# Kernel optimization log

Hardware: AMD Instinct MI355X
Metric: run time of the kernel (lower is better)

The kernel has to match this reference:

```python
import jax, jax.numpy as jnp
import numpy as np

HEADS, LEVELS, POINTS, DIMS = 8, 4, 4, 256
CH = DIMS // HEADS
SHAPES = np.array([[96, 96], [48, 48], [24, 24], [12, 12]], dtype=np.int64)
LEVEL_START = np.concatenate([[0], np.cumsum(SHAPES[:, 0] * SHAPES[:, 1])[:-1]]).astype(np.int64)
HW = int((SHAPES[:, 0] * SHAPES[:, 1]).sum())
N, Q = 2, HW


def setup_inputs() -> dict:
    key = jax.random.key(0)
    ks = jax.random.split(key, 8)
    return {
        "q": jax.random.normal(ks[0], (N, Q, DIMS), jnp.float32),
        "p": jax.random.uniform(ks[1], (N, Q, LEVELS, 2), jnp.float32),
        "v": jax.random.normal(ks[2], (N, HW, DIMS), jnp.float32),
        "W_off": jax.random.normal(ks[3], (DIMS, HEADS * LEVELS * POINTS * 2), jnp.float32) * 0.01,
        "b_off": jax.random.normal(ks[4], (HEADS * LEVELS * POINTS * 2,), jnp.float32) * 0.5,
        "W_attn": jax.random.normal(ks[5], (DIMS, HEADS * LEVELS * POINTS), jnp.float32) * 0.02,
        "b_attn": jnp.zeros((HEADS * LEVELS * POINTS,), jnp.float32),
        "W_in": jax.random.normal(ks[6], (DIMS, DIMS), jnp.float32) / np.float32(np.sqrt(DIMS)),
        "b_in": jnp.zeros((DIMS,), jnp.float32),
        "W_out": jax.random.normal(ks[7], (DIMS, DIMS), jnp.float32) / np.float32(np.sqrt(DIMS)),
        "b_out": jnp.zeros((DIMS,), jnp.float32),
        "shapes": jnp.asarray(SHAPES),
        "level_index": jnp.asarray(LEVEL_START),
    }


def _sample_level(vl, loc_l, Hl, Wl):
    """Bilinear sample with zero padding outside the feature map.
    vl: [N, Hl*Wl, heads, C]; loc_l: [N, Q, heads, P, 2] normalized (x, y) in [0,1].
    Returns [N, Q, P, heads, C]."""
    Nb, Qn, Hd, P, _ = loc_l.shape
    x = loc_l[..., 0] * Wl - 0.5  # pixel coords, align_corners=False convention
    y = loc_l[..., 1] * Hl - 0.5
    x0 = jnp.floor(x)
    y0 = jnp.floor(y)
    dx = x - x0
    dy = y - y0
    x0i = x0.astype(jnp.int32)
    y0i = y0.astype(jnp.int32)
    out = jnp.zeros((Nb, Qn, P, Hd, vl.shape[-1]), vl.dtype)
    corners = ((x0i, y0i, (1 - dx) * (1 - dy)), (x0i + 1, y0i, dx * (1 - dy)),
               (x0i, y0i + 1, (1 - dx) * dy), (x0i + 1, y0i + 1, dx * dy))
    for cx, cy, w in corners:
        valid = (cx >= 0) & (cx < Wl) & (cy >= 0) & (cy < Hl)
        idx = jnp.clip(cy, 0, Hl - 1) * Wl + jnp.clip(cx, 0, Wl - 1)  # [N,Q,Hd,P]
        idx_t = idx.transpose(0, 1, 3, 2).reshape(Nb, Qn * P, Hd, 1)
        g = jnp.take_along_axis(vl, idx_t, axis=1).reshape(Nb, Qn, P, Hd, -1)
        wv = jnp.where(valid, w, 0.0).transpose(0, 1, 3, 2)  # [N,Q,P,Hd]
        out = out + g * wv[..., None].astype(vl.dtype)
    return out


def _forward(q, p, v, W_off, b_off, W_attn, b_attn, W_in, b_in, W_out, b_out, shp, lsi):
    Nb, Qn, _ = q.shape
    v = (v @ W_in + b_in).reshape(Nb, -1, HEADS, CH)
    off = (q @ W_off + b_off).reshape(Nb, Qn, HEADS, LEVELS, POINTS, 2)
    attn = jax.nn.softmax((q @ W_attn + b_attn).reshape(Nb, Qn, HEADS, LEVELS * POINTS), axis=-1)
    attn = attn.reshape(Nb, Qn, HEADS, LEVELS, POINTS)
    # offsets normalized by (W, H) of each level, added to reference points (2-coord branch)
    off_norm = jnp.asarray(np.stack([shp[:, 1], shp[:, 0]], -1), q.dtype)  # [L, 2]
    loc = p[:, :, None, :, None, :] + off / off_norm[None, None, None, :, None, :]  # [N,Q,Hd,L,P,2]
    out = jnp.zeros((Nb, Qn, HEADS, CH), q.dtype)
    for l in range(LEVELS):
        Hl, Wl = int(shp[l, 0]), int(shp[l, 1])
        s = int(lsi[l])
        vl = jax.lax.slice_in_dim(v, s, s + Hl * Wl, axis=1)
        samp = _sample_level(vl, loc[:, :, :, l], Hl, Wl)  # [N,Q,P,Hd,C]
        out = out + jnp.einsum('nqphc,nqhp->nqhc', samp, attn[:, :, :, l])
    return out.reshape(Nb, Qn, DIMS) @ W_out + b_out


def reference(q, p, v, W_off, b_off, W_attn, b_attn, W_in, b_in, W_out, b_out, shapes, level_index):
    shp = np.asarray(shapes)  # spatial shapes are structural constants
    lsi = np.asarray(level_index)
    return _forward(q, p, v, W_off, b_off, W_attn, b_attn, W_in, b_in, W_out, b_out, shp, lsi)
```

## Files before the change

kernel.cpp:

```cpp
#include <hip/hip_runtime.h>
#include <hip/hip_bf16.h>
#include <hip/hip_fp16.h>
#include <math.h>

#define NB      2
#define QN      12240
#define HW_TOT  12240
#define DIMS    256
#define HEADS   8
#define CH      32
#define LEVELS  4
#define POINTS  4
#define M_TOT   (NB * QN)

typedef unsigned short ushort_t;
typedef __attribute__((ext_vector_type(8))) short short8;
typedef __attribute__((ext_vector_type(4))) float floatx4;

__device__ __forceinline__ ushort_t f2bf(float f) {
    __hip_bfloat16 h = __float2bfloat16(f);
    return *reinterpret_cast<ushort_t*>(&h);
}
__device__ __forceinline__ ushort_t f2h(float f) {
    __half h = __float2half(f);
    return *reinterpret_cast<ushort_t*>(&h);
}

__global__ __launch_bounds__(256) void convert_prep_kernel(
    const float* __restrict__ v, const float* __restrict__ q,
    ushort_t* __restrict__ vbf, ushort_t* __restrict__ qbf,
    const float* __restrict__ W_in, const float* __restrict__ W_off,
    const float* __restrict__ W_attn, const float* __restrict__ W_out,
    const float* __restrict__ b_off, const float* __restrict__ b_attn,
    ushort_t* __restrict__ Tin, ushort_t* __restrict__ Tcomb,
    ushort_t* __restrict__ Tout, float* __restrict__ bcomb,
    int* __restrict__ vpad)
{
    const int bx  = blockIdx.x;
    const int tid = threadIdx.x;
    if (bx < 6120) {
        const size_t i = ((size_t)bx * 256 + tid) * 8;
        const size_t half = (size_t)M_TOT * DIMS;
        const float* src; ushort_t* dst; size_t off;
        if (i < half) { src = v; dst = vbf; off = i; }
        else          { src = q; dst = qbf; off = i - half; }
        const float4 a = *(const float4*)&src[off];
        const float4 b = *(const float4*)&src[off + 4];
        ushort_t t[8] = {f2bf(a.x), f2bf(a.y), f2bf(a.z), f2bf(a.w),
                         f2bf(b.x), f2bf(b.y), f2bf(b.z), f2bf(b.w)};
        *(int4*)&dst[off] = *(int4*)t;
        return;
    }
    const int bi = bx - 6120;
    const int gi = bi * 256 + tid;
    if (gi < 32)  vpad[gi] = 0;
    if (gi < 384) bcomb[gi] = (gi < 256) ? b_off[gi] : b_attn[gi - 256];
    const int k = gi & 255;
    const int n = gi >> 8;
    if (gi < 65536) {
        Tin[n * 256 + k]  = f2bf(W_in[k * 256 + n]);
        Tout[n * 256 + k] = f2bf(W_out[k * 256 + n]);
    }
    {
        const float val = (n < 256) ? W_off[k * 256 + n]
                                    : W_attn[k * 128 + (n - 256)];
        Tcomb[n * 256 + k] = f2bf(val);
    }
}

__device__ __forceinline__ void gemm_tile_core(
    const ushort_t* __restrict__ A, const ushort_t* __restrict__ BT,
    const float* __restrict__ bias, void* __restrict__ C, int cmode,
    int M, int Nc, int bm0, int bn0, int K,
    ushort_t* As, ushort_t* Bs)
{
    const int tid  = threadIdx.x;
    const int wave = tid >> 6;
    const int lane = tid & 63;
    const int quad = lane >> 4;
    const int l16  = lane & 15;
    const int wm   = (wave >> 1) * 64;
    const int wn   = (wave & 1) * 64;

    const int off0 = tid * 16;
    const int row0 = off0 >> 6;
    const int kc0  = (off0 & 63) >> 1;

    int ar0 = bm0 + row0;      if (ar0 > M - 1) ar0 = M - 1;
    int ar1 = bm0 + row0 + 64; if (ar1 > M - 1) ar1 = M - 1;

    const ushort_t* ga0 = A  + (size_t)ar0 * K + kc0;
    const ushort_t* ga1 = A  + (size_t)ar1 * K + kc0;
    const ushort_t* gb0 = BT + (size_t)(bn0 + row0) * K + kc0;
    const ushort_t* gb1 = BT + (size_t)(bn0 + row0 + 64) * K + kc0;

    ushort_t* lA0 = As + wave * 512;
    ushort_t* lA1 = As + wave * 512 + 2048;
    ushort_t* lB0 = Bs + wave * 512;
    ushort_t* lB1 = Bs + wave * 512 + 2048;

    floatx4 acc[4][4];
    #pragma unroll
    for (int i = 0; i < 4; ++i)
        #pragma unroll
        for (int j = 0; j < 4; ++j)
            acc[i][j] = (floatx4){0.f, 0.f, 0.f, 0.f};

    for (int kk = 0; kk < K; kk += 32) {
        __builtin_amdgcn_global_load_lds(
            (const __attribute__((address_space(1))) void*)(ga0 + kk),
            (__attribute__((address_space(3))) void*)lA0, 16, 0, 0);
        __builtin_amdgcn_global_load_lds(
            (const __attribute__((address_space(1))) void*)(ga1 + kk),
            (__attribute__((address_space(3))) void*)lA1, 16, 0, 0);
        __builtin_amdgcn_global_load_lds(
            (const __attribute__((address_space(1))) void*)(gb0 + kk),
            (__attribute__((address_space(3))) void*)lB0, 16, 0, 0);
        __builtin_amdgcn_global_load_lds(
            (const __attribute__((address_space(1))) void*)(gb1 + kk),
            (__attribute__((address_space(3))) void*)lB1, 16, 0, 0);
        __syncthreads();

        short8 af[4], bfr[4];
        #pragma unroll
        for (int mt = 0; mt < 4; ++mt)
            af[mt] = *(const short8*)&As[(wm + mt * 16 + l16) * 32 + quad * 8];
        #pragma unroll
        for (int nt = 0; nt < 4; ++nt)
            bfr[nt] = *(const short8*)&Bs[(wn + nt * 16 + l16) * 32 + quad * 8];
        #pragma unroll
        for (int mt = 0; mt < 4; ++mt)
            #pragma unroll
            for (int nt = 0; nt < 4; ++nt)
                acc[mt][nt] = __builtin_amdgcn_mfma_f32_16x16x32_bf16(
                    af[mt], bfr[nt], acc[mt][nt], 0, 0, 0);
        __syncthreads();
    }

    #pragma unroll
    for (int mt = 0; mt < 4; ++mt) {
        #pragma unroll
        for (int j = 0; j < 4; ++j) {
            const int row = bm0 + wm + mt * 16 + quad * 4 + j;
            if (row >= M) continue;
            #pragma unroll
            for (int nt = 0; nt < 4; ++nt) {
                const int col = bn0 + wn + nt * 16 + l16;
                const float val = acc[mt][nt][j] + bias[col];
                if (cmode == 1) {
                    const size_t idx = (((size_t)(col >> 5) * M + row) << 5) + (col & 31);
                    ((ushort_t*)C)[idx] = f2bf(val);
                } else if (cmode == 2) {
                    ((ushort_t*)C)[(size_t)row * Nc + col] = f2h(val);
                } else {
                    ((float*)C)[(size_t)row * Nc + col] = val;
                }
            }
        }
    }
}

__global__ __launch_bounds__(256) void gemm_proj_kernel(
    const ushort_t* __restrict__ vbf, const ushort_t* __restrict__ qbf,
    const ushort_t* __restrict__ Tin, const ushort_t* __restrict__ Tcomb,
    const float* __restrict__ b_in, const float* __restrict__ bcomb,
    ushort_t* __restrict__ vproj, ushort_t* __restrict__ offh)
{
    __shared__ ushort_t As[128 * 32];
    __shared__ ushort_t Bs[128 * 32];
    const int bm0 = blockIdx.x * 128;
    const int y = blockIdx.y;
    if (y < 2)
        gemm_tile_core(vbf, Tin, b_in, vproj, 1, M_TOT, 256, bm0, y * 128, 256, As, Bs);
    else
        gemm_tile_core(qbf, Tcomb, bcomb, offh, 2, M_TOT, 384, bm0, (y - 2) * 128, 256, As, Bs);
}

__global__ __launch_bounds__(256) void gemm_out_kernel(
    const ushort_t* __restrict__ mid, const ushort_t* __restrict__ Tout,
    const float* __restrict__ b_out, float* __restrict__ out)
{
    __shared__ ushort_t As[128 * 32];
    __shared__ ushort_t Bs[128 * 32];
    gemm_tile_core(mid, Tout, b_out, out, 0, M_TOT, 256,
                   blockIdx.x * 128, blockIdx.y * 128, 256, As, Bs);
}

#define LO32(u) __uint_as_float((u) << 16)
#define HI32(u) __uint_as_float((u) & 0xffff0000u)
#define ACC8(W, g) \
    a0 = fmaf(W, LO32(g.x), a0);  a1 = fmaf(W, HI32(g.x), a1); \
    a2 = fmaf(W, LO32(g.y), a2);  a3 = fmaf(W, HI32(g.y), a3); \
    a4 = fmaf(W, LO32(g.z), a4);  a5 = fmaf(W, HI32(g.z), a5); \
    a6 = fmaf(W, LO32(g.w), a6);  a7 = fmaf(W, HI32(g.w), a7);

__global__ __launch_bounds__(256, 8) void msda_sample_kernel(
    const ushort_t* __restrict__ vproj, const ushort_t* __restrict__ offh,
    const float* __restrict__ p, ushort_t* __restrict__ mid)
{
    __shared__ int4 s_main[4][68];
    __shared__ int2 s_aux[4][68];

    const int tid = threadIdx.x;
    const int wv  = tid >> 6;
    const int l   = tid & 63;
    const int idx = blockIdx.x;
    const int b8  = idx & 7;
    const int hh  = b8 >> 2;
    const int qg  = (idx >> 3) * 4 + (b8 & 3);
    const int nq  = qg * 4 + wv;
    const int nb  = (nq >= QN) ? 1 : 0;

    const size_t orow = (size_t)nq * 384;
    const __half2 o2 = *(const __half2*)&offh[orow + hh * 128 + 2 * l];
    const float2  of = __half22float2(o2);
    const float   lg = __half2float(
        *(const __half*)&offh[orow + 256 + hh * 64 + l]);
    const int     lvl = (l >> 2) & 3;
    const float2  pl  = *(const float2*)&p[(size_t)nq * 8 + lvl * 2];

    float mx = lg;
    #pragma unroll
    for (int m = 8; m; m >>= 1) mx = fmaxf(mx, __shfl_xor(mx, m));
    const float e = __expf(lg - mx);
    float ss = e;
    #pragma unroll
    for (int m = 8; m; m >>= 1) ss += __shfl_xor(ss, m);
    const float wt = e * __builtin_amdgcn_rcpf(ss);

    const int   Wl = 96 >> lvl;
    const float fW = (float)Wl;
    const int   st = 12288 - (12288 >> (2 * lvl));
    const int   h4 = l >> 4;
    const int   h  = hh * 4 + h4;

    {
        const float x  = fmaf(pl.x, fW, of.x) - 0.5f;
        const float y  = fmaf(pl.y, fW, of.y) - 0.5f;
        const float xf = floorf(x), yf = floorf(y);
        const float dx = x - xf,    dy = y - yf;
        const int   x0 = (int)xf,   y0 = (int)yf;
        const bool vxl = (unsigned)x0       < (unsigned)Wl;
        const bool vxr = (unsigned)(x0 + 1) < (unsigned)Wl;
        const bool vy0 = (unsigned)y0       < (unsigned)Wl;
        const bool vy1 = (unsigned)(y0 + 1) < (unsigned)Wl;

        const float wxl = vxl ? (1.0f - dx) : (vxr ? dx : 0.0f);
        const float wxr = (vxl && vxr) ? dx : 0.0f;
        const int   xb  = vxl ? x0 : 0;

        const float wy0f = wt * (1.0f - dy), wy1f = wt * dy;
        const float w_l0 = vy0 ? wxl * wy0f : 0.0f;
        const float w_r0 = vy0 ? wxr * wy0f : 0.0f;
        const float w_l1 = vy1 ? wxl * wy1f : 0.0f;
        const float w_r1 = vy1 ? wxr * wy1f : 0.0f;

        int yc0 = y0;     if (yc0 < 0) yc0 = 0; if (yc0 > Wl - 1) yc0 = Wl - 1;
        int yc1 = y0 + 1; if (yc1 < 0) yc1 = 0; if (yc1 > Wl - 1) yc1 = Wl - 1;

        const int rowb = h * M_TOT + nb * HW_TOT + st + xb;
        const int lin0 = rowb + yc0 * Wl;
        const int lin1 = rowb + yc1 * Wl;
        const int e17 = h4 * 17 + (l & 15);
        s_main[wv][e17] = (int4){lin0 << 6, __float_as_int(w_l0),
                                 __float_as_int(w_r0), lin1 << 6};
        s_aux[wv][e17]  = (int2){__float_as_int(w_l1), __float_as_int(w_r1)};
    }

    __builtin_amdgcn_wave_barrier();
    asm volatile("s_waitcnt lgkmcnt(0)" ::: "memory");
    __builtin_amdgcn_wave_barrier();

    const int hg     = l >> 4;
    const int rowr   = (l >> 3) & 1;
    const int corner = (l >> 2) & 1;
    const int c16    = (l & 7) * 16;
    const char* __restrict__ vb = (const char*)vproj;

    float a0 = 0.f, a1 = 0.f, a2 = 0.f, a3 = 0.f;
    float a4 = 0.f, a5 = 0.f, a6 = 0.f, a7 = 0.f;

    #pragma unroll 4
    for (int t = 0; t < 16; ++t) {
        const int  e17 = hg * 17 + t;
        const int4 c   = s_main[wv][e17];
        const int2 cb  = s_aux[wv][e17];
        const int  base = rowr ? c.w : c.x;
        const float wl  = rowr ? __int_as_float(cb.x) : __int_as_float(c.y);
        const float wr  = rowr ? __int_as_float(cb.y) : __int_as_float(c.z);
        const float w   = corner ? wr : wl;
        const uint4 g   = *(const uint4*)(vb + (unsigned)(base + c16));
        ACC8(w, g);
    }

    a0 += __shfl_xor(a0, 4);  a1 += __shfl_xor(a1, 4);
    a2 += __shfl_xor(a2, 4);  a3 += __shfl_xor(a3, 4);
    a4 += __shfl_xor(a4, 4);  a5 += __shfl_xor(a5, 4);
    a6 += __shfl_xor(a6, 4);  a7 += __shfl_xor(a7, 4);
    a0 += __shfl_xor(a0, 8);  a1 += __shfl_xor(a1, 8);
    a2 += __shfl_xor(a2, 8);  a3 += __shfl_xor(a3, 8);
    a4 += __shfl_xor(a4, 8);  a5 += __shfl_xor(a5, 8);
    a6 += __shfl_xor(a6, 8);  a7 += __shfl_xor(a7, 8);

    if ((l & 12) == 0) {
        ushort_t mv[8] = {f2bf(a0), f2bf(a1), f2bf(a2), f2bf(a3),
                          f2bf(a4), f2bf(a5), f2bf(a6), f2bf(a7)};
        const int col = (hh * 4 + hg) * 32 + (l & 3) * 8;
        *(uint4*)&mid[(size_t)nq * 256 + col] = *(uint4*)mv;
    }
}

extern "C" void kernel_launch(void* const* d_in, const int* in_sizes, int n_in,
                              void* d_out, int out_size, void* d_ws, size_t ws_size,
                              hipStream_t stream)
{
    const float* q      = (const float*)d_in[0];
    const float* p      = (const float*)d_in[1];
    const float* v      = (const float*)d_in[2];
    const float* W_off  = (const float*)d_in[3];
    const float* b_off  = (const float*)d_in[4];
    const float* W_attn = (const float*)d_in[5];
    const float* b_attn = (const float*)d_in[6];
    const float* W_in   = (const float*)d_in[7];
    const float* b_in   = (const float*)d_in[8];
    const float* W_out  = (const float*)d_in[9];
    const float* b_out  = (const float*)d_in[10];
    float* out = (float*)d_out;

    const int M = M_TOT;

    ushort_t* vproj  = (ushort_t*)d_ws;
    ushort_t* vpad   = vproj + (size_t)M * 256;
    ushort_t* offh   = vpad + 64;
    ushort_t* vbf    = offh + (size_t)M * 384;
    ushort_t* mid    = vbf;
    ushort_t* qbf    = vbf + (size_t)M * 256;
    ushort_t* Tin    = qbf + (size_t)M * 256;
    ushort_t* Tcomb  = Tin + 256 * 256;
    ushort_t* Tout   = Tcomb + 384 * 256;
    float*    bcomb  = (float*)(Tout + 256 * 256);

    convert_prep_kernel<<<dim3(6504), 256, 0, stream>>>(
        v, q, vbf, qbf, W_in, W_off, W_attn, W_out, b_off, b_attn,
        Tin, Tcomb, Tout, bcomb, (int*)vpad);

    gemm_proj_kernel<<<dim3(192, 5), 256, 0, stream>>>(
        vbf, qbf, Tin, Tcomb, b_in, bcomb, vproj, offh);
    msda_sample_kernel<<<dim3(12240), 256, 0, stream>>>(vproj, offh, p, mid);
    gemm_out_kernel<<<dim3(192, 2), 256, 0, stream>>>(mid, Tout, b_out, out);
}
```

Measured before the change: 179.9 us.

## Fuse fp32-to-bf16 activation conversion into projection GEMM with dual-N tiles

Removes the separate pass that converted v and q to bf16 and instead loads fp32 activations directly in the projection GEMM, converting them in registers before writing them to LDS. Each block now also computes two 128-column N tiles from one converted A tile, so the A conversion and loads are shared across 256 output columns. This cuts a full write and reread of the bf16 copies and reduces the grid from 5 to 3 column groups. In exchange the fp32 A loads double the A read bytes per block and are synchronous register loads rather than async LDS loads, and the dual accumulators raise register pressure.

Measured after the change: 178.1 us. Within noise of the previous version (-1.0%).

```diff
diff --git a/kernel.cpp b/kernel.cpp
--- a/kernel.cpp
+++ b/kernel.cpp
@@ -26,9 +26,7 @@
     return *reinterpret_cast<ushort_t*>(&h);
 }
 
-__global__ __launch_bounds__(256) void convert_prep_kernel(
-    const float* __restrict__ v, const float* __restrict__ q,
-    ushort_t* __restrict__ vbf, ushort_t* __restrict__ qbf,
+__global__ __launch_bounds__(256) void prep_weights_kernel(
     const float* __restrict__ W_in, const float* __restrict__ W_off,
     const float* __restrict__ W_attn, const float* __restrict__ W_out,
     const float* __restrict__ b_off, const float* __restrict__ b_attn,
@@ -36,23 +34,7 @@
     ushort_t* __restrict__ Tout, float* __restrict__ bcomb,
     int* __restrict__ vpad)
 {
-    const int bx  = blockIdx.x;
-    const int tid = threadIdx.x;
-    if (bx < 6120) {
-        const size_t i = ((size_t)bx * 256 + tid) * 8;
-        const size_t half = (size_t)M_TOT * DIMS;
-        const float* src; ushort_t* dst; size_t off;
-        if (i < half) { src = v; dst = vbf; off = i; }
-        else          { src = q; dst = qbf; off = i - half; }
-        const float4 a = *(const float4*)&src[off];
-        const float4 b = *(const float4*)&src[off + 4];
-        ushort_t t[8] = {f2bf(a.x), f2bf(a.y), f2bf(a.z), f2bf(a.w),
-                         f2bf(b.x), f2bf(b.y), f2bf(b.z), f2bf(b.w)};
-        *(int4*)&dst[off] = *(int4*)t;
-        return;
-    }
-    const int bi = bx - 6120;
-    const int gi = bi * 256 + tid;
+    const int gi = blockIdx.x * 256 + threadIdx.x;
     if (gi < 32)  vpad[gi] = 0;
     if (gi < 384) bcomb[gi] = (gi < 256) ? b_off[gi] : b_attn[gi - 256];
     const int k = gi & 255;
@@ -61,18 +43,17 @@
         Tin[n * 256 + k]  = f2bf(W_in[k * 256 + n]);
         Tout[n * 256 + k] = f2bf(W_out[k * 256 + n]);
     }
-    {
-        const float val = (n < 256) ? W_off[k * 256 + n]
-                                    : W_attn[k * 128 + (n - 256)];
-        Tcomb[n * 256 + k] = f2bf(val);
-    }
-}
-
-__device__ __forceinline__ void gemm_tile_core(
-    const ushort_t* __restrict__ A, const ushort_t* __restrict__ BT,
-    const float* __restrict__ bias, void* __restrict__ C, int cmode,
-    int M, int Nc, int bm0, int bn0, int K,
-    ushort_t* As, ushort_t* Bs)
+    const float val = (n < 256) ? W_off[k * 256 + n]
+                                : W_attn[k * 128 + (n - 256)];
+    Tcomb[n * 256 + k] = f2bf(val);
+}
+
+template<int CMODE, bool DUAL>
+__device__ __forceinline__ void gemm_fused_tile(
+    const float* __restrict__ A32, const ushort_t* __restrict__ BT,
+    const float* __restrict__ bias, void* __restrict__ C,
+    int M, int Nc, int bm0, int bn0a, int bn0b,
+    ushort_t* As, ushort_t* Bs0, ushort_t* Bs1)
 {
     const int tid  = threadIdx.x;
     const int wave = tid >> 6;
@@ -89,6 +70,152 @@
     int ar0 = bm0 + row0;      if (ar0 > M - 1) ar0 = M - 1;
     int ar1 = bm0 + row0 + 64; if (ar1 > M - 1) ar1 = M - 1;
 
+    const float*    gA0  = A32 + (size_t)ar0 * 256 + kc0;
+    const float*    gA1  = A32 + (size_t)ar1 * 256 + kc0;
+    const ushort_t* gb0a = BT + (size_t)(bn0a + row0) * 256 + kc0;
+    const ushort_t* gb1a = BT + (size_t)(bn0a + row0 + 64) * 256 + kc0;
+    const ushort_t* gb0b = BT + (size_t)(bn0b + row0) * 256 + kc0;
+    const ushort_t* gb1b = BT + (size_t)(bn0b + row0 + 64) * 256 + kc0;
+
+    ushort_t* lB0a = Bs0 + wave * 512;
+    ushort_t* lB1a = Bs0 + wave * 512 + 2048;
+    ushort_t* lB0b = Bs1 + wave * 512;
+    ushort_t* lB1b = Bs1 + wave * 512 + 2048;
+
+    floatx4 acc0[4][4], acc1[4][4];
+    #pragma unroll
+    for (int i = 0; i < 4; ++i)
+        #pragma unroll
+        for (int j = 0; j < 4; ++j) {
+            acc0[i][j] = (floatx4){0.f, 0.f, 0.f, 0.f};
+            if (DUAL) acc1[i][j] = (floatx4){0.f, 0.f, 0.f, 0.f};
+        }
+
+    for (int kk = 0; kk < 256; kk += 32) {
+        __builtin_amdgcn_global_load_lds(
+            (const __attribute__((address_space(1))) void*)(gb0a + kk),
+            (__attribute__((address_space(3))) void*)lB0a, 16, 0, 0);
+        __builtin_amdgcn_global_load_lds(
+            (const __attribute__((address_space(1))) void*)(gb1a + kk),
+            (__attribute__((address_space(3))) void*)lB1a, 16, 0, 0);
+        if (DUAL) {
+            __builtin_amdgcn_global_load_lds(
+                (const __attribute__((address_space(1))) void*)(gb0b + kk),
+                (__attribute__((address_space(3))) void*)lB0b, 16, 0, 0);
+            __builtin_amdgcn_global_load_lds(
+                (const __attribute__((address_space(1))) void*)(gb1b + kk),
+                (__attribute__((address_space(3))) void*)lB1b, 16, 0, 0);
+        }
+        {
+            const float4 a0 = *(const float4*)(gA0 + kk);
+            const float4 a1 = *(const float4*)(gA0 + kk + 4);
+            const float4 b0 = *(const float4*)(gA1 + kk);
+            const float4 b1 = *(const float4*)(gA1 + kk + 4);
+            ushort_t t0[8] = {f2bf(a0.x), f2bf(a0.y), f2bf(a0.z), f2bf(a0.w),
+                              f2bf(a1.x), f2bf(a1.y), f2bf(a1.z), f2bf(a1.w)};
+            ushort_t t1[8] = {f2bf(b0.x), f2bf(b0.y), f2bf(b0.z), f2bf(b0.w),
+                              f2bf(b1.x), f2bf(b1.y), f2bf(b1.z), f2bf(b1.w)};
+            *(int4*)&As[tid * 8]        = *(int4*)t0;
+            *(int4*)&As[tid * 8 + 2048] = *(int4*)t1;
+        }
+        __syncthreads();
+
+        short8 af[4], bfa[4], bfb[4];
+        #pragma unroll
+        for (int mt = 0; mt < 4; ++mt)
+            af[mt] = *(const short8*)&As[(wm + mt * 16 + l16) * 32 + quad * 8];
+        #pragma unroll
+        for (int nt = 0; nt < 4; ++nt) {
+            bfa[nt] = *(const short8*)&Bs0[(wn + nt * 16 + l16) * 32 + quad * 8];
+            if (DUAL)
+                bfb[nt] = *(const short8*)&Bs1[(wn + nt * 16 + l16) * 32 + quad * 8];
+        }
+        #pragma unroll
+        for (int mt = 0; mt < 4; ++mt)
+            #pragma unroll
+            for (int nt = 0; nt < 4; ++nt) {
+                acc0[mt][nt] = __builtin_amdgcn_mfma_f32_16x16x32_bf16(
+                    af[mt], bfa[nt], acc0[mt][nt], 0, 0, 0);
+                if (DUAL)
+                    acc1[mt][nt] = __builtin_amdgcn_mfma_f32_16x16x32_bf16(
+                        af[mt], bfb[nt], acc1[mt][nt], 0, 0, 0);
+            }
+        __syncthreads();
+    }
+
+    #pragma unroll
+    for (int mt = 0; mt < 4; ++mt) {
+        #pragma unroll
+        for (int j = 0; j < 4; ++j) {
+            const int row = bm0 + wm + mt * 16 + quad * 4 + j;
+            if (row >= M) continue;
+            #pragma unroll
+            for (int nt = 0; nt < 4; ++nt) {
+                {
+                    const int col = bn0a + wn + nt * 16 + l16;
+                    const float val = acc0[mt][nt][j] + bias[col];
+                    if (CMODE == 1) {
+                        const size_t idx = (((size_t)(col >> 5) * M + row) << 5) + (col & 31);
+                        ((ushort_t*)C)[idx] = f2bf(val);
+                    } else {
+                        ((ushort_t*)C)[(size_t)row * Nc + col] = f2h(val);
+                    }
+                }
+                if (DUAL) {
+                    const int col = bn0b + wn + nt * 16 + l16;
+                    const float val = acc1[mt][nt][j] + bias[col];
+                    if (CMODE == 1) {
+                        const size_t idx = (((size_t)(col >> 5) * M + row) << 5) + (col & 31);
+                        ((ushort_t*)C)[idx] = f2bf(val);
+                    } else {
+                        ((ushort_t*)C)[(size_t)row * Nc + col] = f2h(val);
+                    }
+                }
+            }
+        }
+    }
+}
+
+__global__ __launch_bounds__(256) void gemm_proj_kernel(
+    const float* __restrict__ v, const float* __restrict__ q,
+    const ushort_t* __restrict__ Tin, const ushort_t* __restrict__ Tcomb,
+    const float* __restrict__ b_in, const float* __restrict__ bcomb,
+    ushort_t* __restrict__ vproj, ushort_t* __restrict__ offh)
+{
+    __shared__ ushort_t As [128 * 32];
+    __shared__ ushort_t Bs0[128 * 32];
+    __shared__ ushort_t Bs1[128 * 32];
+    const int bm0 = blockIdx.x * 128;
+    const int y = blockIdx.y;
+    if (y == 0)
+        gemm_fused_tile<1, true >(v, Tin,   b_in,  vproj, M_TOT, 256, bm0, 0, 128, As, Bs0, Bs1);
+    else if (y == 1)
+        gemm_fused_tile<2, true >(q, Tcomb, bcomb, offh,  M_TOT, 384, bm0, 0, 128, As, Bs0, Bs1);
+    else
+        gemm_fused_tile<2, false>(q, Tcomb, bcomb, offh,  M_TOT, 384, bm0, 256, 0, As, Bs0, Bs1);
+}
+
+__device__ __forceinline__ void gemm_tile_core(
+    const ushort_t* __restrict__ A, const ushort_t* __restrict__ BT,
+    const float* __restrict__ bias, float* __restrict__ C,
+    int M, int Nc, int bm0, int bn0, int K,
+    ushort_t* As, ushort_t* Bs)
+{
+    const int tid  = threadIdx.x;
+    const int wave = tid >> 6;
+    const int lane = tid & 63;
+    const int quad = lane >> 4;
+    const int l16  = lane & 15;
+    const int wm   = (wave >> 1) * 64;
+    const int wn   = (wave & 1) * 64;
+
+    const int off0 = tid * 16;
+    const int row0 = off0 >> 6;
+    const int kc0  = (off0 & 63) >> 1;
+
+    int ar0 = bm0 + row0;      if (ar0 > M - 1) ar0 = M - 1;
+    int ar1 = bm0 + row0 + 64; if (ar1 > M - 1) ar1 = M - 1;
+
     const ushort_t* ga0 = A  + (size_t)ar0 * K + kc0;
     const ushort_t* ga1 = A  + (size_t)ar1 * K + kc0;
     const ushort_t* gb0 = BT + (size_t)(bn0 + row0) * K + kc0;
@@ -146,34 +273,10 @@
             #pragma unroll
             for (int nt = 0; nt < 4; ++nt) {
                 const int col = bn0 + wn + nt * 16 + l16;
-                const float val = acc[mt][nt][j] + bias[col];
-                if (cmode == 1) {
-                    const size_t idx = (((size_t)(col >> 5) * M + row) << 5) + (col & 31);
-                    ((ushort_t*)C)[idx] = f2bf(val);
-                } else if (cmode == 2) {
-                    ((ushort_t*)C)[(size_t)row * Nc + col] = f2h(val);
-                } else {
-                    ((float*)C)[(size_t)row * Nc + col] = val;
-                }
+                C[(size_t)row * Nc + col] = acc[mt][nt][j] + bias[col];
             }
         }
     }
-}
-
-__global__ __launch_bounds__(256) void gemm_proj_kernel(
-    const ushort_t* __restrict__ vbf, const ushort_t* __restrict__ qbf,
-    const ushort_t* __restrict__ Tin, const ushort_t* __restrict__ Tcomb,
-    const float* __restrict__ b_in, const float* __restrict__ bcomb,
-    ushort_t* __restrict__ vproj, ushort_t* __restrict__ offh)
-{
-    __shared__ ushort_t As[128 * 32];
-    __shared__ ushort_t Bs[128 * 32];
-    const int bm0 = blockIdx.x * 128;
-    const int y = blockIdx.y;
-    if (y < 2)
-        gemm_tile_core(vbf, Tin, b_in, vproj, 1, M_TOT, 256, bm0, y * 128, 256, As, Bs);
-    else
-        gemm_tile_core(qbf, Tcomb, bcomb, offh, 2, M_TOT, 384, bm0, (y - 2) * 128, 256, As, Bs);
 }
 
 __global__ __launch_bounds__(256) void gemm_out_kernel(
@@ -182,7 +285,7 @@
 {
     __shared__ ushort_t As[128 * 32];
     __shared__ ushort_t Bs[128 * 32];
-    gemm_tile_core(mid, Tout, b_out, out, 0, M_TOT, 256,
+    gemm_tile_core(mid, Tout, b_out, out, M_TOT, 256,
                    blockIdx.x * 128, blockIdx.y * 128, 256, As, Bs);
 }
 
@@ -332,20 +435,18 @@
     ushort_t* vproj  = (ushort_t*)d_ws;
     ushort_t* vpad   = vproj + (size_t)M * 256;
     ushort_t* offh   = vpad + 64;
-    ushort_t* vbf    = offh + (size_t)M * 384;
-    ushort_t* mid    = vbf;
-    ushort_t* qbf    = vbf + (size_t)M * 256;
-    ushort_t* Tin    = qbf + (size_t)M * 256;
+    ushort_t* mid    = offh + (size_t)M * 384;
+    ushort_t* Tin    = mid + (size_t)M * 256;
     ushort_t* Tcomb  = Tin + 256 * 256;
     ushort_t* Tout   = Tcomb + 384 * 256;
     float*    bcomb  = (float*)(Tout + 256 * 256);
 
-    convert_prep_kernel<<<dim3(6504), 256, 0, stream>>>(
-        v, q, vbf, qbf, W_in, W_off, W_attn, W_out, b_off, b_attn,
+    prep_weights_kernel<<<dim3(384), 256, 0, stream>>>(
+        W_in, W_off, W_attn, W_out, b_off, b_attn,
         Tin, Tcomb, Tout, bcomb, (int*)vpad);
 
-    gemm_proj_kernel<<<dim3(192, 5), 256, 0, stream>>>(
-        vbf, qbf, Tin, Tcomb, b_in, bcomb, vproj, offh);
+    gemm_proj_kernel<<<dim3(192, 3), 256, 0, stream>>>(
+        v, q, Tin, Tcomb, b_in, bcomb, vproj, offh);
     msda_sample_kernel<<<dim3(12240), 256, 0, stream>>>(vproj, offh, p, mid);
     gemm_out_kernel<<<dim3(192, 2), 256, 0, stream>>>(mid, Tout, b_out, out);
 }
```
